# Kernel tuning notes

Measured on AMD Instinct MI355X. Metric: run time of the kernel, lower is better.

The kernel has to match this reference:

```python
import jax, jax.numpy as jnp
import numpy as np

N = 10000   # nodes
D = 256     # in_channels
E = 8192    # target edges
OUT = 1     # out_channels
P_EDGE = 0.003  # ~30 avg degree


def setup_inputs() -> dict:
    key = jax.random.key(0)
    k1, k2, k3, k4 = jax.random.split(key, 4)
    x = jax.random.normal(k1, (N, D), dtype=jnp.float32)
    adj1 = jax.random.bernoulli(k2, P_EDGE, (N, N))          # 1-hop adjacency (bool)
    adj01 = adj1 | jnp.eye(N, dtype=bool)                    # hop 0+1 (adds self-loops)
    tar_ei = jax.random.randint(k3, (2, E), 0, N)
    Wxs = jax.random.normal(k4, (OUT, 3 * D), dtype=jnp.float32) * 0.02
    bxs = jnp.zeros((OUT,), dtype=jnp.float32)
    return {"x": x, "adj01": adj01, "adj1": adj1, "tar_ei": tar_ei,
            "Wxs": Wxs, "bxs": bxs, "NCN_mode": 0}


def reference(x, adj01, adj1, tar_ei, Wxs, bxs, NCN_mode):
    # NCN_mode == 0 branch of multidomainforward (k = 3)
    ti, tj = tar_ei[0], tar_ei[1]
    xij = x[ti] * x[tj]                                      # [E, D]
    # adjoverlap: common-neighbor indicator per target edge  [E, N]
    cn01 = adj01[ti] & adj01[tj]
    cn1 = adj1[ti] & adj1[tj]
    # sparse_diff: neighbors common at hop{0,1} but not hop 1
    cn0 = cn01 & (~cn1)
    # spmm_add: sum features over common neighbors
    xcn0 = cn0.astype(x.dtype) @ x                           # [E, D]
    xcn1 = cn1.astype(x.dtype) @ x                           # [E, D]
    xs = jnp.concatenate([xij, xcn0, xcn1], axis=-1)         # [E, 3D]
    # note: original `xs.relu()` is non-in-place and discarded -> no relu
    return xs @ Wxs.T + bxs                                  # [E, OUT]
```

## Files before the change

### kernel.cpp

```cpp
#include <hip/hip_runtime.h>

#define NN        10000
#define D_IN      256
#define EE        8192
#define GROUPS    157
#define ROW_U64   160
#define UNITS     1250

typedef unsigned long long u64;

__device__ __forceinline__ bool probe_is_byte(const unsigned char* adj01_bytes) {
    return adj01_bytes[10001] != 0;
}

__global__ void node_kernel(const float* __restrict__ x,
                            const float* __restrict__ W,
                            const void* __restrict__ adj1,
                            const unsigned char* __restrict__ adj01_bytes,
                            float* __restrict__ y1,
                            float* __restrict__ y2,
                            u64* __restrict__ p1) {
    const int n = blockIdx.x, tid = threadIdx.x;

    const float p = x[(size_t)n * D_IN + tid];
    float s1 = p * W[D_IN + tid];
    float s2 = p * W[2 * D_IN + tid];
    #pragma unroll
    for (int off = 32; off > 0; off >>= 1) {
        s1 += __shfl_down(s1, off);
        s2 += __shfl_down(s2, off);
    }
    __shared__ float q1[4], q2[4];
    const int lane = tid & 63, wid = tid >> 6;
    if (lane == 0) { q1[wid] = s1; q2[wid] = s2; }

    unsigned char* drow = (unsigned char*)(p1 + (size_t)n * ROW_U64);
    if (probe_is_byte(adj01_bytes)) {
        const u64* src = (const u64*)((const unsigned char*)adj1 + (size_t)n * NN);
        #pragma unroll 5
        for (int u = tid; u < UNITS; u += 256) {
            const u64 v = src[u];
            unsigned m = 0;
            #pragma unroll
            for (int b = 0; b < 8; ++b)
                m |= ((v >> (8 * b)) & 0xFFull) ? (1u << b) : 0u;
            drow[u] = (unsigned char)m;
        }
    } else {
        const uint4* src = (const uint4*)((const int*)adj1 + (size_t)n * NN);
        #pragma unroll 5
        for (int u = tid; u < UNITS; u += 256) {
            const uint4 a = src[2 * u], b = src[2 * u + 1];
            const unsigned m = (a.x ? 1u : 0u) | (a.y ? 2u : 0u) | (a.z ? 4u : 0u) |
                               (a.w ? 8u : 0u) | (b.x ? 16u : 0u) | (b.y ? 32u : 0u) |
                               (b.z ? 64u : 0u) | (b.w ? 128u : 0u);
            drow[u] = (unsigned char)m;
        }
    }
    for (int b = UNITS + tid; b < ROW_U64 * 8; b += 256) drow[b] = 0;

    __syncthreads();
    if (tid == 0) {
        y1[n] = q1[0] + q1[1] + q1[2] + q1[3];
        y2[n] = q2[0] + q2[1] + q2[2] + q2[3];
    }
}

__global__ void edge_packed_kernel(const float* __restrict__ x,
                                   const int* __restrict__ tar,
                                   const float* __restrict__ W,
                                   const float* __restrict__ bxs,
                                   const float* __restrict__ y1,
                                   const float* __restrict__ y2,
                                   const u64* __restrict__ p1,
                                   float* __restrict__ out) {
    const int e = blockIdx.x, tid = threadIdx.x;
    const int ti = tar[e], tj = tar[EE + e];

    float acc = x[(size_t)ti * D_IN + tid] * x[(size_t)tj * D_IN + tid] * W[tid];

    if (tid < GROUPS) {
        u64 c1 = p1[(size_t)ti * ROW_U64 + tid] & p1[(size_t)tj * ROW_U64 + tid];
        const int base = tid * 64;
        while (c1) { acc += y2[base + __builtin_ctzll(c1)]; c1 &= c1 - 1; }
    }

    if (tid == 0) {
        #define BIT(r, c) ((int)((p1[(size_t)(r) * ROW_U64 + ((c) >> 6)] >> ((c) & 63)) & 1ull))
        if (ti != tj) {
            if (BIT(ti, tj) && !BIT(tj, tj)) acc += y1[tj];
            if (BIT(tj, ti) && !BIT(ti, ti)) acc += y1[ti];
        } else {
            if (!BIT(ti, ti)) acc += y1[ti];
        }
        #undef BIT
    }

    #pragma unroll
    for (int off = 32; off > 0; off >>= 1) acc += __shfl_down(acc, off);
    __shared__ float part[4];
    const int lane = tid & 63, wid = tid >> 6;
    if (lane == 0) part[wid] = acc;
    __syncthreads();
    if (tid == 0) out[e] = part[0] + part[1] + part[2] + part[3] + bxs[0];
}

__global__ void edge_direct_kernel(const float* __restrict__ x,
                                   const void* __restrict__ adj1,
                                   const unsigned char* __restrict__ adj01_bytes,
                                   const int* __restrict__ tar,
                                   const float* __restrict__ W,
                                   const float* __restrict__ bxs,
                                   const float* __restrict__ y1,
                                   const float* __restrict__ y2,
                                   float* __restrict__ out) {
    const int e = blockIdx.x, tid = threadIdx.x;
    const int ti = tar[e], tj = tar[EE + e];
    const bool isByte = probe_is_byte(adj01_bytes);
    float acc = x[(size_t)ti * D_IN + tid] * x[(size_t)tj * D_IN + tid] * W[tid];

    #define AD(r, c) (isByte ? (((const unsigned char*)adj1)[(size_t)(r) * NN + (c)] != 0) \
                             : (((const int*)adj1)[(size_t)(r) * NN + (c)] != 0))
    for (int n = tid; n < NN; n += 256)
        if (AD(ti, n) && AD(tj, n)) acc += y2[n];
    if (tid == 0) {
        if (ti != tj) {
            if (AD(ti, tj) && !AD(tj, tj)) acc += y1[tj];
            if (AD(tj, ti) && !AD(ti, ti)) acc += y1[ti];
        } else if (!AD(ti, ti)) acc += y1[ti];
    }
    #undef AD

    #pragma unroll
    for (int off = 32; off > 0; off >>= 1) acc += __shfl_down(acc, off);
    __shared__ float part[4];
    const int lane = tid & 63, wid = tid >> 6;
    if (lane == 0) part[wid] = acc;
    __syncthreads();
    if (tid == 0) out[e] = part[0] + part[1] + part[2] + part[3] + bxs[0];
}

extern "C" void kernel_launch(void* const* d_in, const int* in_sizes, int n_in,
                              void* d_out, int out_size, void* d_ws, size_t ws_size,
                              hipStream_t stream) {
    const float*         x     = (const float*)d_in[0];
    const unsigned char* adj01 = (const unsigned char*)d_in[1];
    const void*          adj1  = d_in[2];
    const int*           tar   = (const int*)d_in[3];
    const float*         W     = (const float*)d_in[4];
    const float*         bxs   = (const float*)d_in[5];

    float* y1 = (float*)d_ws;
    float* y2 = y1 + NN;
    u64*   p1 = (u64*)((char*)d_ws + ((2 * NN * sizeof(float) + 255) & ~255ull));
    const size_t need = ((2 * NN * sizeof(float) + 255) & ~255ull)
                      + (size_t)NN * ROW_U64 * sizeof(u64);

    float* out = (float*)d_out;

    if (ws_size >= need) {
        node_kernel<<<NN, 256, 0, stream>>>(x, W, adj1, adj01, y1, y2, p1);
        edge_packed_kernel<<<EE, 256, 0, stream>>>(x, tar, W, bxs, y1, y2, p1, out);
    } else {
        node_kernel<<<NN, 256, 0, stream>>>(x, W, adj1, adj01, y1, y2, (u64*)y1 );
        edge_direct_kernel<<<EE, 256, 0, stream>>>(x, adj1, adj01, tar, W, bxs, y1, y2, out);
    }
}
```

Before: 683.5 us.

## Pack only adjacency rows referenced by target edges, one wave per row

Adds a mark kernel that flags every node appearing in tar_ei. The node kernel then bit-packs adjacency rows only for flagged nodes, since the edge kernel only reads packed rows of its two endpoints. The node kernel now handles four rows per block, one wave per row. It uses float4 loads for the projections and writes 32-bit mask words built from eight uint4 loads per lane, replacing byte writes. This cuts adjacency read traffic and per-row block overhead, at the cost of an extra memset and a small launch, plus an unpacked tail in rows that are skipped.

```diff
diff --git a/kernel.cpp b/kernel.cpp
--- a/kernel.cpp
+++ b/kernel.cpp
@@ -5,65 +5,94 @@
 #define EE        8192
 #define GROUPS    157
 #define ROW_U64   160
-#define UNITS     1250
+#define UNITS4    312
 
 typedef unsigned long long u64;
 
 __device__ __forceinline__ bool probe_is_byte(const unsigned char* adj01_bytes) {
     return adj01_bytes[10001] != 0;
+}
+
+__global__ void mark_kernel(const int* __restrict__ tar,
+                            unsigned char* __restrict__ rowmask) {
+    const int i = blockIdx.x * 256 + threadIdx.x;
+    if (i < 2 * EE) rowmask[tar[i]] = 1;
 }
 
 __global__ void node_kernel(const float* __restrict__ x,
                             const float* __restrict__ W,
                             const void* __restrict__ adj1,
                             const unsigned char* __restrict__ adj01_bytes,
+                            const unsigned char* __restrict__ rowmask,
                             float* __restrict__ y1,
                             float* __restrict__ y2,
                             u64* __restrict__ p1) {
-    const int n = blockIdx.x, tid = threadIdx.x;
-
-    const float p = x[(size_t)n * D_IN + tid];
-    float s1 = p * W[D_IN + tid];
-    float s2 = p * W[2 * D_IN + tid];
+    const int lane = threadIdx.x & 63, wave = threadIdx.x >> 6;
+    const int row = blockIdx.x * 4 + wave;
+
+    const float4 xv = ((const float4*)(x + (size_t)row * D_IN))[lane];
+    const float4 w1 = ((const float4*)(W + D_IN))[lane];
+    const float4 w2 = ((const float4*)(W + 2 * D_IN))[lane];
+    float s1 = xv.x * w1.x + xv.y * w1.y + xv.z * w1.z + xv.w * w1.w;
+    float s2 = xv.x * w2.x + xv.y * w2.y + xv.z * w2.z + xv.w * w2.w;
     #pragma unroll
     for (int off = 32; off > 0; off >>= 1) {
         s1 += __shfl_down(s1, off);
         s2 += __shfl_down(s2, off);
     }
-    __shared__ float q1[4], q2[4];
-    const int lane = tid & 63, wid = tid >> 6;
-    if (lane == 0) { q1[wid] = s1; q2[wid] = s2; }
-
-    unsigned char* drow = (unsigned char*)(p1 + (size_t)n * ROW_U64);
-    if (probe_is_byte(adj01_bytes)) {
-        const u64* src = (const u64*)((const unsigned char*)adj1 + (size_t)n * NN);
-        #pragma unroll 5
-        for (int u = tid; u < UNITS; u += 256) {
-            const u64 v = src[u];
-            unsigned m = 0;
-            #pragma unroll
-            for (int b = 0; b < 8; ++b)
-                m |= ((v >> (8 * b)) & 0xFFull) ? (1u << b) : 0u;
-            drow[u] = (unsigned char)m;
+    if (lane == 0) { y1[row] = s1; y2[row] = s2; }
+
+    if (!rowmask[row]) return;
+
+    unsigned char* drow = (unsigned char*)(p1 + (size_t)row * ROW_U64);
+    unsigned* drow32 = (unsigned*)drow;
+
+    if (!probe_is_byte(adj01_bytes)) {
+        const uint4* src = (const uint4*)((const int*)adj1 + (size_t)row * NN);
+        for (int u = lane; u < UNITS4; u += 64) {
+            uint4 q[8];
+            #pragma unroll
+            for (int k = 0; k < 8; ++k) q[k] = src[u * 8 + k];
+            unsigned m = 0;
+            #pragma unroll
+            for (int k = 0; k < 8; ++k) {
+                m |= (q[k].x ? 1u : 0u) << (4 * k + 0);
+                m |= (q[k].y ? 1u : 0u) << (4 * k + 1);
+                m |= (q[k].z ? 1u : 0u) << (4 * k + 2);
+                m |= (q[k].w ? 1u : 0u) << (4 * k + 3);
+            }
+            drow32[u] = m;
+        }
+        if (lane < 2) {
+            const int* s32 = (const int*)adj1 + (size_t)row * NN + 9984 + lane * 8;
+            unsigned m = 0;
+            #pragma unroll
+            for (int b = 0; b < 8; ++b) m |= (s32[b] ? 1u : 0u) << b;
+            drow[1248 + lane] = (unsigned char)m;
         }
     } else {
-        const uint4* src = (const uint4*)((const int*)adj1 + (size_t)n * NN);
-        #pragma unroll 5
-        for (int u = tid; u < UNITS; u += 256) {
-            const uint4 a = src[2 * u], b = src[2 * u + 1];
-            const unsigned m = (a.x ? 1u : 0u) | (a.y ? 2u : 0u) | (a.z ? 4u : 0u) |
-                               (a.w ? 8u : 0u) | (b.x ? 16u : 0u) | (b.y ? 32u : 0u) |
-                               (b.z ? 64u : 0u) | (b.w ? 128u : 0u);
-            drow[u] = (unsigned char)m;
-        }
-    }
-    for (int b = UNITS + tid; b < ROW_U64 * 8; b += 256) drow[b] = 0;
-
-    __syncthreads();
-    if (tid == 0) {
-        y1[n] = q1[0] + q1[1] + q1[2] + q1[3];
-        y2[n] = q2[0] + q2[1] + q2[2] + q2[3];
-    }
+        const uint4* src = (const uint4*)((const unsigned char*)adj1 + (size_t)row * NN);
+        for (int u = lane; u < UNITS4; u += 64) {
+            const uint4 a = src[u * 2], b = src[u * 2 + 1];
+            unsigned m = 0;
+            const unsigned w[8] = { a.x, a.y, a.z, a.w, b.x, b.y, b.z, b.w };
+            #pragma unroll
+            for (int k = 0; k < 8; ++k) {
+                #pragma unroll
+                for (int j = 0; j < 4; ++j)
+                    m |= (((w[k] >> (8 * j)) & 0xFFu) ? 1u : 0u) << (4 * k + j);
+            }
+            drow32[u] = m;
+        }
+        if (lane < 2) {
+            const unsigned char* s8 = (const unsigned char*)adj1 + (size_t)row * NN + 9984 + lane * 8;
+            unsigned m = 0;
+            #pragma unroll
+            for (int b = 0; b < 8; ++b) m |= (s8[b] ? 1u : 0u) << b;
+            drow[1248 + lane] = (unsigned char)m;
+        }
+    }
+    if (lane >= 2 && lane < 32) drow[1248 + lane] = 0;
 }
 
 __global__ void edge_packed_kernel(const float* __restrict__ x,
@@ -150,19 +179,25 @@
     const float*         W     = (const float*)d_in[4];
     const float*         bxs   = (const float*)d_in[5];
 
-    float* y1 = (float*)d_ws;
-    float* y2 = y1 + NN;
-    u64*   p1 = (u64*)((char*)d_ws + ((2 * NN * sizeof(float) + 255) & ~255ull));
-    const size_t need = ((2 * NN * sizeof(float) + 255) & ~255ull)
+    float*         y1      = (float*)d_ws;
+    float*         y2      = y1 + NN;
+    unsigned char* rowmask = (unsigned char*)(y2 + NN);
+    u64*           p1      = (u64*)((char*)d_ws +
+                              ((2 * NN * sizeof(float) + NN + 255) & ~(size_t)255));
+    const size_t need = ((2 * NN * sizeof(float) + NN + 255) & ~(size_t)255)
                       + (size_t)NN * ROW_U64 * sizeof(u64);
 
     float* out = (float*)d_out;
 
     if (ws_size >= need) {
-        node_kernel<<<NN, 256, 0, stream>>>(x, W, adj1, adj01, y1, y2, p1);
+        hipMemsetAsync(rowmask, 0, NN, stream);
+        mark_kernel<<<(2 * EE + 255) / 256, 256, 0, stream>>>(tar, rowmask);
+        node_kernel<<<NN / 4, 256, 0, stream>>>(x, W, adj1, adj01, rowmask, y1, y2, p1);
         edge_packed_kernel<<<EE, 256, 0, stream>>>(x, tar, W, bxs, y1, y2, p1, out);
     } else {
-        node_kernel<<<NN, 256, 0, stream>>>(x, W, adj1, adj01, y1, y2, (u64*)y1 );
+        hipMemsetAsync(rowmask, 1, NN, stream);
+        node_kernel<<<NN / 4, 256, 0, stream>>>(x, W, adj1, adj01, rowmask, y1, y2,
+                                                (u64*)y1 );
         edge_direct_kernel<<<EE, 256, 0, stream>>>(x, adj1, adj01, tar, W, bxs, y1, y2, out);
     }
 }
```

Result: no change. 696.6 us (+1.9%).
